# Kernel optimization log

Measured on AMD Instinct MI355X. Metric: run time of the kernel, lower is better.

The kernel has to match this reference:

```python
import jax, jax.numpy as jnp
import numpy as np

B, H, W = 32, 56, 56
C_IN, C_OUT, GROUPS, K = 256, 256, 32, 3
EPS = 1e-5


def setup_inputs() -> dict:
    key = jax.random.key(0)
    k1, k2 = jax.random.split(key, 2)
    x = jax.random.normal(k1, (B, H, W, C_IN), dtype=jnp.float32)
    # HWIO grouped-conv kernel: I = C_IN // GROUPS = 8; equivalent to the
    # concatenation of the 32 per-group [3,3,8,8] Conv2d kernels along O.
    w = jax.random.normal(k2, (K, K, C_IN // GROUPS, C_OUT), dtype=jnp.float32) * 0.05
    b = jnp.zeros((C_OUT,), dtype=jnp.float32)
    gamma = jnp.ones((C_OUT,), dtype=jnp.float32)
    beta = jnp.zeros((C_OUT,), dtype=jnp.float32)
    return {"x": x, "w": w, "b": b, "gamma": gamma, "beta": beta}


def reference(x, w, b, gamma, beta):
    # Grouped conv: same math as tf.split -> per-group Conv2d -> tf.concat,
    # expressed as one native grouped convolution (feature_group_count).
    y = jax.lax.conv_general_dilated(
        x, w,
        window_strides=(1, 1),
        padding="SAME",
        dimension_numbers=("NHWC", "HWIO", "NHWC"),
        feature_group_count=GROUPS,
    ) + b  # [B,H,W,C_OUT]
    # BatchNorm (training forward: batch statistics over N,H,W per channel)
    mean = jnp.mean(y, axis=(0, 1, 2))
    var = jnp.var(y, axis=(0, 1, 2))
    y = (y - mean) * jax.lax.rsqrt(var + EPS) * gamma + beta
    # Act('relu')
    return jax.nn.relu(y)
```

## Files before the change

### kernel.cpp

```cpp
#include <hip/hip_runtime.h>
#include <hip/hip_bf16.h>

#define BB 32
#define HH 56
#define WW 56
#define CC 256
#define NPIX (BB*HH*WW)
#define EPS 1e-5f

typedef short bf16x8 __attribute__((ext_vector_type(8)));
typedef float f32x4  __attribute__((ext_vector_type(4)));

__device__ __forceinline__ unsigned short f2bf(float f) {
    __hip_bfloat16 h = __float2bfloat16(f);
    return *reinterpret_cast<unsigned short*>(&h);
}


__global__ void k0_zero(float* stats) { stats[threadIdx.x] = 0.f; }

__global__ __launch_bounds__(256, 5) void k1_conv(
    const float* __restrict__ x, const float* __restrict__ wgt,
    __hip_bfloat16* __restrict__ y, float* __restrict__ stats)
{
    __shared__ unsigned short xt[10*58*24];
    __shared__ float bsum[16], bsq[16];

    const int gp = blockIdx.x;
    const int hb = blockIdx.y;
    const int b  = blockIdx.z;
    const int t  = threadIdx.x;
    const int h0 = hb * 8;

    if (t < 16) { bsum[t] = 0.f; bsq[t] = 0.f; }

    float4 v[10];
    int    off[10];
    #pragma unroll
    for (int j = 0; j < 10; ++j) {
        const int i   = j*256 + t;
        const int ci4 = i & 3;
        const int cq  = i >> 2;
        const int row = cq / 58;
        const int col = cq - row*58;
        const int hh  = h0 - 1 + row;
        const int wc  = col - 1;
        off[j] = (row*58 + col)*24 + ci4*4;
        v[j] = make_float4(0.f, 0.f, 0.f, 0.f);
        if (i < 2320 && (unsigned)hh < HH && (unsigned)wc < WW)
            v[j] = *(const float4*)(x + (((size_t)(b*HH + hh)*WW + wc)*CC + gp*16 + ci4*4));
    }
    #pragma unroll
    for (int j = 0; j < 10; ++j) {
        if (j*256 + t < 2320) {
            ushort4 s;
            s.x = f2bf(v[j].x); s.y = f2bf(v[j].y);
            s.z = f2bf(v[j].z); s.w = f2bf(v[j].w);
            *(ushort4*)(xt + off[j]) = s;
        }
    }

    const int lane = t & 63;
    const int rp   = t >> 6;
    const int n    = lane & 15;
    const int q    = lane >> 4;

    bf16x8 wfrag[5];
    #pragma unroll
    for (int s = 0; s < 5; ++s) {
        const int o   = s*4 + q;
        const int g   = (o >= 10);
        const int tap = o - g*10;
        bf16x8 f = {0,0,0,0,0,0,0,0};
        if (tap < 9 && (n >> 3) == g) {
            #pragma unroll
            for (int e = 0; e < 8; ++e)
                f[e] = (short)f2bf(wgt[(tap*8 + e)*CC + gp*16 + n]);
        }
        wfrag[s] = f;
    }

    __syncthreads();

    const int m    = lane & 15;
    const int rowr = rp*2 + (m >> 3);
    const int colb = m & 7;

    int aoff[5];
    #pragma unroll
    for (int s = 0; s < 5; ++s) {
        int o  = s*4 + q;
        int g  = (o >= 10);
        int tp = o - g*10;
        if (tp == 9) tp = 0;
        int dh = tp / 3, dw = tp - dh*3;
        aoff[s] = ((rowr + dh)*58 + colb + dw)*24 + g*8;
    }

    const int h = h0 + rowr;
    const size_t pixbase = ((size_t)(b*HH + h))*WW;
    float lsum[4] = {0.f, 0.f, 0.f, 0.f};
    float lsq[4]  = {0.f, 0.f, 0.f, 0.f};

    #pragma unroll 2
    for (int ct = 0; ct < 7; ++ct) {
        f32x4 acc = {0.f, 0.f, 0.f, 0.f};
        #pragma unroll
        for (int s = 0; s < 5; ++s) {
            bf16x8 af = *(const bf16x8*)(xt + aoff[s] + ct*192);
            acc = __builtin_amdgcn_mfma_f32_16x16x32_bf16(wfrag[s], af, acc, 0, 0, 0);
        }
        ushort4 st;
        st.x = f2bf(acc[0]); st.y = f2bf(acc[1]);
        st.z = f2bf(acc[2]); st.w = f2bf(acc[3]);
        *(ushort4*)(y + (pixbase + ct*8 + colb)*CC + gp*16 + q*4) = st;
        #pragma unroll
        for (int i = 0; i < 4; ++i) {
            lsum[i] += acc[i];
            lsq[i]  += acc[i]*acc[i];
        }
    }

    #pragma unroll
    for (int d = 8; d >= 1; d >>= 1) {
        #pragma unroll
        for (int i = 0; i < 4; ++i) {
            lsum[i] += __shfl_xor(lsum[i], d);
            lsq[i]  += __shfl_xor(lsq[i],  d);
        }
    }
    if (m == 0) {
        #pragma unroll
        for (int i = 0; i < 4; ++i) {
            atomicAdd(&bsum[q*4 + i], lsum[i]);
            atomicAdd(&bsq[q*4 + i],  lsq[i]);
        }
    }
    __syncthreads();
    if (t < 16) {
        atomicAdd(&stats[gp*16 + t],       bsum[t]);
        atomicAdd(&stats[256 + gp*16 + t], bsq[t]);
    }
}

__global__ void k2_finalize(const float* __restrict__ stats,
                            const float* __restrict__ gamma,
                            const float* __restrict__ beta,
                            float* __restrict__ ss)
{
    int c = threadIdx.x;
    float inv_n = 1.f / (float)NPIX;
    float mean = stats[c] * inv_n;
    float var  = stats[256 + c] * inv_n - mean * mean;
    float scale = gamma[c] * rsqrtf(var + EPS);
    ss[c]       = scale;
    ss[256 + c] = beta[c] - mean * scale;
}

__global__ __launch_bounds__(256) void k3_norm(
    const __hip_bfloat16* __restrict__ y, const float* __restrict__ ss,
    float* __restrict__ out)
{
    const int t   = threadIdx.x;
    const int oct = t & 31;
    const int pr  = t >> 5;
    const int c0  = oct * 8;

    float4 sc0 = *(const float4*)(ss + c0);
    float4 sc1 = *(const float4*)(ss + c0 + 4);
    float4 sh0 = *(const float4*)(ss + 256 + c0);
    float4 sh1 = *(const float4*)(ss + 256 + c0 + 4);

    const uint4* yv = (const uint4*)y;
    float4* ov = (float4*)out;
    const int px0 = blockIdx.x * 32 + pr;

    uint4 d[4];
    #pragma unroll
    for (int i = 0; i < 4; ++i)
        d[i] = yv[(size_t)(px0 + i*8)*32 + oct];

    #pragma unroll
    for (int i = 0; i < 4; ++i) {
        const int px = px0 + i*8;
        float f0 = __uint_as_float((d[i].x & 0xffffu) << 16);
        float f1 = __uint_as_float(d[i].x & 0xffff0000u);
        float f2 = __uint_as_float((d[i].y & 0xffffu) << 16);
        float f3 = __uint_as_float(d[i].y & 0xffff0000u);
        float f4 = __uint_as_float((d[i].z & 0xffffu) << 16);
        float f5 = __uint_as_float(d[i].z & 0xffff0000u);
        float f6 = __uint_as_float((d[i].w & 0xffffu) << 16);
        float f7 = __uint_as_float(d[i].w & 0xffff0000u);

        float4 o0, o1;
        o0.x = fmaxf(0.f, f0 * sc0.x + sh0.x);
        o0.y = fmaxf(0.f, f1 * sc0.y + sh0.y);
        o0.z = fmaxf(0.f, f2 * sc0.z + sh0.z);
        o0.w = fmaxf(0.f, f3 * sc0.w + sh0.w);
        o1.x = fmaxf(0.f, f4 * sc1.x + sh1.x);
        o1.y = fmaxf(0.f, f5 * sc1.y + sh1.y);
        o1.z = fmaxf(0.f, f6 * sc1.z + sh1.z);
        o1.w = fmaxf(0.f, f7 * sc1.w + sh1.w);

        ov[(size_t)px*64 + oct*2]     = o0;
        ov[(size_t)px*64 + oct*2 + 1] = o1;
    }
}

extern "C" void kernel_launch(void* const* d_in, const int* in_sizes, int n_in,
                              void* d_out, int out_size, void* d_ws, size_t ws_size,
                              hipStream_t stream) {
    const float* x     = (const float*)d_in[0];
    const float* wgt   = (const float*)d_in[1];
    const float* gamma = (const float*)d_in[3];
    const float* beta  = (const float*)d_in[4];
    float* out = (float*)d_out;

    float* stats = (float*)d_ws;
    float* ss    = (float*)((char*)d_ws + 2048);
    __hip_bfloat16* y = (__hip_bfloat16*)((char*)d_ws + 4096);

    k0_zero<<<1, 512, 0, stream>>>(stats);
    k1_conv<<<dim3(16, 7, BB), 256, 0, stream>>>(x, wgt, y, stats);
    k2_finalize<<<1, 256, 0, stream>>>(stats, gamma, beta, ss);
    k3_norm<<<NPIX/32, 256, 0, stream>>>(y, ss, out);
}
```

Measured before the change: 247.2 us.

## Pre-convert input to bf16 group-major layout before grouped conv

Adds a pre-pass kernel that converts the fp32 NHWC input to bf16 and transposes it into a group-major layout, with 8 contiguous channels per pixel per group. The conv kernel then loads 16-byte bf16 chunks per pixel-group instead of strided fp32 float4 loads, and no longer converts in its own load phase. This reduces the conv's read traffic and gives it contiguous per-group access, at the cost of an extra full read of x plus a write and re-read of the bf16 copy, and an extra launch.

```diff
diff --git a/kernel.cpp b/kernel.cpp
--- a/kernel.cpp
+++ b/kernel.cpp
@@ -6,6 +6,8 @@
 #define WW 56
 #define CC 256
 #define NPIX (BB*HH*WW)
+#define GRP 32
+#define GSZ (NPIX*8)
 #define EPS 1e-5f
 
 typedef short bf16x8 __attribute__((ext_vector_type(8)));
@@ -19,8 +21,39 @@
 
 __global__ void k0_zero(float* stats) { stats[threadIdx.x] = 0.f; }
 
+__global__ __launch_bounds__(256) void k_pre(
+    const float* __restrict__ x, __hip_bfloat16* __restrict__ xg)
+{
+    __shared__ unsigned short lx[32*260];
+    const int t  = threadIdx.x;
+    const int P0 = blockIdx.x * 32;
+
+    #pragma unroll
+    for (int r = 0; r < 8; ++r) {
+        const int id  = r*256 + t;
+        const int pix = id >> 6;
+        const int c4  = id & 63;
+        float4 v = *(const float4*)(x + (size_t)(P0+pix)*CC + c4*4);
+        ushort4 s;
+        s.x = f2bf(v.x); s.y = f2bf(v.y); s.z = f2bf(v.z); s.w = f2bf(v.w);
+        *(ushort4*)(lx + pix*260 + c4*4) = s;
+    }
+    __syncthreads();
+    #pragma unroll
+    for (int r = 0; r < 4; ++r) {
+        const int oid = r*256 + t;
+        const int pl  = oid & 31;
+        const int g   = oid >> 5;
+        ushort4 a = *(const ushort4*)(lx + pl*260 + g*8);
+        ushort4 c = *(const ushort4*)(lx + pl*260 + g*8 + 4);
+        __hip_bfloat16* dst = xg + (size_t)g*GSZ + (size_t)(P0+pl)*8;
+        *(ushort4*)dst       = a;
+        *(ushort4*)(dst + 4) = c;
+    }
+}
+
 __global__ __launch_bounds__(256, 5) void k1_conv(
-    const float* __restrict__ x, const float* __restrict__ wgt,
+    const __hip_bfloat16* __restrict__ xg, const float* __restrict__ wgt,
     __hip_bfloat16* __restrict__ y, float* __restrict__ stats)
 {
     __shared__ unsigned short xt[10*58*24];
@@ -34,30 +67,21 @@
 
     if (t < 16) { bsum[t] = 0.f; bsq[t] = 0.f; }
 
-    float4 v[10];
-    int    off[10];
-    #pragma unroll
-    for (int j = 0; j < 10; ++j) {
-        const int i   = j*256 + t;
-        const int ci4 = i & 3;
-        const int cq  = i >> 2;
-        const int row = cq / 58;
-        const int col = cq - row*58;
+    #pragma unroll
+    for (int j = 0; j < 5; ++j) {
+        const int e   = j*256 + t;
+        const int col = e % 58;
+        const int rg  = e / 58;
+        const int row = rg >> 1;
+        const int g   = rg & 1;
         const int hh  = h0 - 1 + row;
         const int wc  = col - 1;
-        off[j] = (row*58 + col)*24 + ci4*4;
-        v[j] = make_float4(0.f, 0.f, 0.f, 0.f);
-        if (i < 2320 && (unsigned)hh < HH && (unsigned)wc < WW)
-            v[j] = *(const float4*)(x + (((size_t)(b*HH + hh)*WW + wc)*CC + gp*16 + ci4*4));
-    }
-    #pragma unroll
-    for (int j = 0; j < 10; ++j) {
-        if (j*256 + t < 2320) {
-            ushort4 s;
-            s.x = f2bf(v[j].x); s.y = f2bf(v[j].y);
-            s.z = f2bf(v[j].z); s.w = f2bf(v[j].w);
-            *(ushort4*)(xt + off[j]) = s;
-        }
+        uint4 v = make_uint4(0u, 0u, 0u, 0u);
+        if (e < 1160 && (unsigned)hh < HH && (unsigned)wc < WW)
+            v = *(const uint4*)(xg + (size_t)(gp*2+g)*GSZ
+                                   + (size_t)((b*HH + hh)*WW + wc)*8);
+        if (e < 1160)
+            *(uint4*)(xt + (row*58 + col)*24 + g*8) = v;
     }
 
     const int lane = t & 63;
@@ -218,10 +242,12 @@
 
     float* stats = (float*)d_ws;
     float* ss    = (float*)((char*)d_ws + 2048);
-    __hip_bfloat16* y = (__hip_bfloat16*)((char*)d_ws + 4096);
+    __hip_bfloat16* y  = (__hip_bfloat16*)((char*)d_ws + 4096);
+    __hip_bfloat16* xg = (__hip_bfloat16*)((char*)d_ws + 4096 + (size_t)NPIX*CC*2);
 
     k0_zero<<<1, 512, 0, stream>>>(stats);
-    k1_conv<<<dim3(16, 7, BB), 256, 0, stream>>>(x, wgt, y, stats);
+    k_pre<<<NPIX/32, 256, 0, stream>>>(x, xg);
+    k1_conv<<<dim3(16, 7, BB), 256, 0, stream>>>(xg, wgt, y, stats);
     k2_finalize<<<1, 256, 0, stream>>>(stats, gamma, beta, ss);
     k3_norm<<<NPIX/32, 256, 0, stream>>>(y, ss, out);
 }
```

Result: slower. 253.3 us (+2.5%).
